# Performance work log

Hardware: AMD Instinct MI355X
Metric: run time of the kernel (lower is better)

Reference implementation:

```python
import jax, jax.numpy as jnp
import numpy as np

NUM_EXPERTS = 8
TOP_K = 2
HIDDEN = 1024
INTER = 1408
B, S = 2, 1024


def setup_inputs() -> dict:
    key = jax.random.key(0)
    k1, k2, k3, k4, k5 = jax.random.split(key, 5)
    scale = 0.02  # keep activations well-scaled
    return {
        "hidden_states": jax.random.normal(k1, (B, S, HIDDEN), dtype=jnp.float32),
        "gate_w": jax.random.normal(k2, (HIDDEN, NUM_EXPERTS), dtype=jnp.float32) * scale,
        "w_gate": jax.random.normal(k3, (NUM_EXPERTS, HIDDEN, INTER), dtype=jnp.float32) * scale,
        "w_up": jax.random.normal(k4, (NUM_EXPERTS, HIDDEN, INTER), dtype=jnp.float32) * scale,
        "w_down": jax.random.normal(k5, (NUM_EXPERTS, INTER, HIDDEN), dtype=jnp.float32) * scale,
    }


def reference(hidden_states, gate_w, w_gate, w_up, w_down):
    b, s, h = hidden_states.shape
    x = hidden_states.reshape(-1, h)  # [T, H]
    # Router: softmax in fp32, top-k, renormalize over selected experts
    logits = x @ gate_w  # [T, E]
    probs = jax.nn.softmax(logits.astype(jnp.float32), axis=-1)
    rw, sel = jax.lax.top_k(probs, TOP_K)  # [T, K]
    rw = rw / jnp.sum(rw, axis=-1, keepdims=True)
    rw = rw.astype(x.dtype)
    # Per-(token, expert) combine weight; duplicates summed (matches torch mask sum)
    combine = jnp.sum(rw[:, :, None] * jax.nn.one_hot(sel, NUM_EXPERTS, dtype=x.dtype), axis=1)  # [T, E]
    out = jnp.zeros_like(x)
    for e in range(NUM_EXPERTS):  # fixed small structural loop over experts
        inter = jax.nn.silu(x @ w_gate[e]) * (x @ w_up[e])  # [T, I]
        out = out + (inter @ w_down[e]) * combine[:, e:e + 1]
    return out.reshape(b, s, h)
```

## Files before the change

### kernel.cpp

```cpp
#include <hip/hip_runtime.h>
#include <hip/hip_bf16.h>

#define T_TOKENS 2048
#define HID 1024
#define ISZ 1408
#define NEXP 8
#define TILES_MAX 72

typedef __bf16 bf16x8 __attribute__((ext_vector_type(8)));
typedef __bf16 bf16x4 __attribute__((ext_vector_type(4)));
typedef float  f32x16 __attribute__((ext_vector_type(16)));

__device__ __forceinline__ void gload16(const void* g, void* l) {
    __builtin_amdgcn_global_load_lds(
        (const __attribute__((address_space(1))) void*)g,
        (__attribute__((address_space(3))) void*)l,
        16, 0, 0);
}

#define PIPE_BARRIER(N)                                              \
    asm volatile("s_waitcnt vmcnt(" #N ") lgkmcnt(0)" ::: "memory"); \
    __builtin_amdgcn_sched_barrier(0);                               \
    __builtin_amdgcn_s_barrier();                                    \
    __builtin_amdgcn_sched_barrier(0);

__global__ __launch_bounds__(256) void prep_kernel(
    const float* __restrict__ x, const float* __restrict__ gw,
    int* __restrict__ sel, float* __restrict__ wt, __bf16* __restrict__ xb,
    const float* __restrict__ wg, const float* __restrict__ wu, const float* __restrict__ wd,
    __bf16* __restrict__ wgT, __bf16* __restrict__ wuT, __bf16* __restrict__ wdT)
{
    __shared__ __bf16 tb[2][64][70];
    const int bid = blockIdx.x;
    const int tid = threadIdx.x;

    if (bid < 512) {
        const int wave = tid >> 6;
        const int lane = tid & 63;
        const int t = bid * 4 + wave;
        const float* xr = x + (size_t)t * HID;

        const int c0 = lane * 16;
        float4 v0 = *(const float4*)(xr + c0);
        float4 v1 = *(const float4*)(xr + c0 + 4);
        float4 v2 = *(const float4*)(xr + c0 + 8);
        float4 v3 = *(const float4*)(xr + c0 + 12);
        {
            bf16x8 o0, o1;
            o0[0]=(__bf16)v0.x; o0[1]=(__bf16)v0.y; o0[2]=(__bf16)v0.z; o0[3]=(__bf16)v0.w;
            o0[4]=(__bf16)v1.x; o0[5]=(__bf16)v1.y; o0[6]=(__bf16)v1.z; o0[7]=(__bf16)v1.w;
            o1[0]=(__bf16)v2.x; o1[1]=(__bf16)v2.y; o1[2]=(__bf16)v2.z; o1[3]=(__bf16)v2.w;
            o1[4]=(__bf16)v3.x; o1[5]=(__bf16)v3.y; o1[6]=(__bf16)v3.z; o1[7]=(__bf16)v3.w;
            *(bf16x8*)(xb + (size_t)t * HID + c0) = o0;
            *(bf16x8*)(xb + (size_t)t * HID + c0 + 8) = o1;
        }
        if (bid == 0 && tid < 128) {
            bf16x8 z8;
            #pragma unroll
            for (int j = 0; j < 8; ++j) z8[j] = (__bf16)0.f;
            *(bf16x8*)(xb + (size_t)T_TOKENS * HID + tid * 8) = z8;
        }

        float le[8] = {0.f, 0.f, 0.f, 0.f, 0.f, 0.f, 0.f, 0.f};
        float xv[16];
        xv[0]=v0.x; xv[1]=v0.y; xv[2]=v0.z; xv[3]=v0.w;
        xv[4]=v1.x; xv[5]=v1.y; xv[6]=v1.z; xv[7]=v1.w;
        xv[8]=v2.x; xv[9]=v2.y; xv[10]=v2.z; xv[11]=v2.w;
        xv[12]=v3.x; xv[13]=v3.y; xv[14]=v3.z; xv[15]=v3.w;
        #pragma unroll
        for (int j = 0; j < 16; ++j) {
            const float* gr = gw + (size_t)(c0 + j) * NEXP;
            float4 g0 = *(const float4*)gr;
            float4 g1 = *(const float4*)(gr + 4);
            le[0] += xv[j] * g0.x; le[1] += xv[j] * g0.y;
            le[2] += xv[j] * g0.z; le[3] += xv[j] * g0.w;
            le[4] += xv[j] * g1.x; le[5] += xv[j] * g1.y;
            le[6] += xv[j] * g1.z; le[7] += xv[j] * g1.w;
        }
        #pragma unroll
        for (int d = 1; d < 64; d <<= 1) {
            #pragma unroll
            for (int k = 0; k < 8; ++k) le[k] += __shfl_xor(le[k], d);
        }
        float m = le[0];
        #pragma unroll
        for (int k = 1; k < 8; ++k) m = fmaxf(m, le[k]);
        float pe[8]; float s = 0.f;
        #pragma unroll
        for (int k = 0; k < 8; ++k) { pe[k] = expf(le[k] - m); s += pe[k]; }
        int e1 = 0; float p1 = pe[0];
        #pragma unroll
        for (int k = 1; k < 8; ++k) if (pe[k] > p1) { p1 = pe[k]; e1 = k; }
        int e2 = -1; float p2 = -1.f;
        #pragma unroll
        for (int k = 0; k < 8; ++k) if (k != e1 && pe[k] > p2) { p2 = pe[k]; e2 = k; }
        if (lane == 0) {
            float inv = 1.0f / (p1 + p2);
            sel[t * 2 + 0] = e1; sel[t * 2 + 1] = e2;
            wt[t * 2 + 0] = p1 * inv; wt[t * 2 + 1] = p2 * inv;
        }
        return;
    }

    const int f   = bid - 512;
    const int z   = f / 176;
    const int rem = f % 176;
    const int bx  = rem / 16;
    const int by  = rem & 15;
    const int e   = z & 7;
    const float* in;
    __bf16* out;
    int R, C, rrA, ccA, rrB, ccB;
    if (z < 16) {
        R = HID; C = ISZ;
        rrA = rrB = by * 64;
        ccA = bx * 128; ccB = ccA + 64;
        in  = (z < 8 ? wg : wu)  + (size_t)e * R * C;
        out = (z < 8 ? wgT : wuT) + (size_t)e * R * C;
    } else {
        R = ISZ; C = HID;
        ccA = ccB = by * 64;
        rrA = bx * 128; rrB = rrA + 64;
        in  = wd  + (size_t)e * R * C;
        out = wdT + (size_t)e * R * C;
    }
    const int lr  = tid >> 4;
    const int lc4 = (tid & 15) * 4;

    auto loadcvt = [&](int buf, int rr, int cc) {
        #pragma unroll
        for (int p = 0; p < 4; ++p) {
            float4 v = *(const float4*)(in + (size_t)(rr + p * 16 + lr) * C + cc + lc4);
            bf16x4 w;
            w[0] = (__bf16)v.x; w[1] = (__bf16)v.y; w[2] = (__bf16)v.z; w[3] = (__bf16)v.w;
            *(bf16x4*)&tb[buf][p * 16 + lr][lc4] = w;
        }
    };
    auto storeT = [&](int buf, int rr, int cc) {
        #pragma unroll
        for (int q = 0; q < 2; ++q) {
            const int oc = (tid >> 3) + 32 * q;
            const int vs = (tid & 7) * 8;
            bf16x8 w;
            #pragma unroll
            for (int j = 0; j < 8; ++j) w[j] = tb[buf][vs + j][oc];
            *(bf16x8*)(out + (size_t)(cc + oc) * R + rr + vs) = w;
        }
    };

    loadcvt(0, rrA, ccA);
    __syncthreads();
    loadcvt(1, rrB, ccB);
    storeT(0, rrA, ccA);
    __syncthreads();
    storeT(1, rrB, ccB);
}

__global__ __launch_bounds__(1024) void scan_assign_kernel(
    int* __restrict__ tiles,
    const int* __restrict__ sel, const float* __restrict__ wt,
    int* __restrict__ rtok, float* __restrict__ rwt, int* __restrict__ tok2row)
{
    __shared__ int hist[NEXP];
    __shared__ int soff[NEXP];
    __shared__ int scur[NEXP];
    if (threadIdx.x < NEXP) { hist[threadIdx.x] = 0; scur[threadIdx.x] = 0; }
    __syncthreads();
    for (int t = threadIdx.x; t < T_TOKENS; t += 1024) {
        atomicAdd(&hist[sel[t * 2 + 0]], 1);
        atomicAdd(&hist[sel[t * 2 + 1]], 1);
    }
    __syncthreads();
    if (threadIdx.x == 0) {
        int cur = 0, tix = 0;
        for (int e = 0; e < NEXP; ++e) {
            soff[e] = cur;
            int n64 = (hist[e] + 63) & ~63;
            for (int rt = 0; rt * 64 < n64; ++rt)
                tiles[tix++] = (e << 16) | (cur + rt * 64);
            cur += n64;
        }
        for (; tix < TILES_MAX; ++tix) tiles[tix] = -1;
    }
    __syncthreads();
    for (int t = threadIdx.x; t < T_TOKENS; t += 1024) {
        #pragma unroll
        for (int k = 0; k < 2; ++k) {
            int e = sel[t * 2 + k];
            int pos = atomicAdd(&scur[e], 1);
            int row = soff[e] + pos;
            rtok[row] = t + 1;
            rwt[row] = wt[t * 2 + k];
            tok2row[t * 2 + k] = row;
        }
    }
}

__global__ __launch_bounds__(256) void ffn1_kernel(
    const __bf16* __restrict__ xb, const int* __restrict__ rtok,
    const __bf16* __restrict__ wgT, const __bf16* __restrict__ wuT,
    const int* __restrict__ tiles, __bf16* __restrict__ inter)
{
    const int n  = blockIdx.x;
    const int nn = (n & 7) * 198 + (n >> 3);
    const int i0 = (nn / TILES_MAX) * 64;
    const int tv = tiles[nn % TILES_MAX];
    if (tv < 0) return;
    const int e = tv >> 16;
    const int rowbase = tv & 0xFFFF;

    __shared__ __align__(16) __bf16 sA[4][64][32];
    __shared__ __align__(16) __bf16 sG[4][64][32];
    __shared__ __align__(16) __bf16 sU[4][64][32];

    const int lane = threadIdx.x & 63;
    const int wid  = threadIdx.x >> 6;
    const int wr = wid >> 1, wc = wid & 1;
    const int l31 = lane & 31;
    const int kg  = lane >> 5;

    const int r16 = lane >> 2;
    const int cz  = (((lane & 3) ^ ((r16 >> 1) & 3)) * 8);
    const int rowA = rowbase + wid * 16 + r16;
    const int tokp = rtok[rowA];
    const int src  = tokp ? (tokp - 1) : T_TOKENS;
    const __bf16* A0 = xb + (size_t)src * HID + cz;
    const size_t wb = (size_t)e * ISZ * HID + (size_t)(i0 + wid * 16 + r16) * HID + cz;
    const __bf16* G0 = wgT + wb;
    const __bf16* U0 = wuT + wb;

    f32x16 accG, accU;
    #pragma unroll
    for (int r = 0; r < 16; ++r) { accG[r] = 0.f; accU[r] = 0.f; }

    auto stage = [&](int b, int k0) {
        gload16(A0 + k0, &sA[b][wid * 16][0]);
        gload16(G0 + k0, &sG[b][wid * 16][0]);
        gload16(U0 + k0, &sU[b][wid * 16][0]);
    };
    auto compute = [&](int b) {
        #pragma unroll
        for (int s = 0; s < 2; ++s) {
            const int ch = ((2 * s + kg) ^ ((l31 >> 1) & 3)) * 8;
            bf16x8 a_ = *(const bf16x8*)&sA[b][wr * 32 + l31][ch];
            bf16x8 g_ = *(const bf16x8*)&sG[b][wc * 32 + l31][ch];
            bf16x8 u_ = *(const bf16x8*)&sU[b][wc * 32 + l31][ch];
            __builtin_amdgcn_s_setprio(1);
            accG = __builtin_amdgcn_mfma_f32_32x32x16_bf16(a_, g_, accG, 0, 0, 0);
            accU = __builtin_amdgcn_mfma_f32_32x32x16_bf16(a_, u_, accU, 0, 0, 0);
            __builtin_amdgcn_s_setprio(0);
        }
    };

    const int nIter = HID / 32;
    stage(0, 0);
    stage(1, 32);
    stage(2, 64);
    PIPE_BARRIER(6)
    for (int i = 0; i < nIter; ++i) {
        int ks = (i + 3 < nIter) ? (i + 3) * 32 : 0;
        stage((i + 3) & 3, ks);
        compute(i & 3);
        PIPE_BARRIER(6)
    }

    const int base_row = rowbase + wr * 32;
    #pragma unroll
    for (int r = 0; r < 16; ++r) {
        float g = accG[r];
        float u = accU[r];
        float v = g / (1.0f + __expf(-g)) * u;
        int row = base_row + (r & 3) + 8 * (r >> 2) + 4 * kg;
        inter[(size_t)row * ISZ + i0 + wc * 32 + l31] = (__bf16)v;
    }
}

__global__ __launch_bounds__(256) void ffn2_kernel(
    const __bf16* __restrict__ inter, const __bf16* __restrict__ wdT,
    const float* __restrict__ rwt, const int* __restrict__ tiles,
    float* __restrict__ y)
{
    const int n  = blockIdx.x;
    const int nn = (n & 7) * 72 + (n >> 3);
    const int n0 = (nn / TILES_MAX) * 128;
    const int tv = tiles[nn % TILES_MAX];
    if (tv < 0) return;
    const int e = tv >> 16;
    const int rowbase = tv & 0xFFFF;

    __shared__ __align__(16) __bf16 sA[4][64][32];
    __shared__ __align__(16) __bf16 sB[4][128][32];

    const int lane = threadIdx.x & 63;
    const int wid  = threadIdx.x >> 6;
    const int wr = wid >> 1, wc = wid & 1;
    const int l31 = lane & 31;
    const int kg  = lane >> 5;

    const int r16 = lane >> 2;
    const int cz  = (((lane & 3) ^ ((r16 >> 1) & 3)) * 8);
    const __bf16* A0 = inter + (size_t)(rowbase + wid * 16 + r16) * ISZ + cz;
    const __bf16* B0 = wdT + (size_t)e * HID * ISZ + (size_t)(n0 + wid * 32 + r16) * ISZ + cz;
    const size_t rstepB = (size_t)16 * ISZ;

    f32x16 acc[2];
    #pragma unroll
    for (int q = 0; q < 2; ++q)
        #pragma unroll
        for (int r = 0; r < 16; ++r) acc[q][r] = 0.f;

    auto stage = [&](int b, int k0) {
        gload16(A0 + k0,          &sA[b][wid * 16][0]);
        gload16(B0 + k0,          &sB[b][wid * 32][0]);
        gload16(B0 + k0 + rstepB, &sB[b][wid * 32 + 16][0]);
    };
    auto compute = [&](int b) {
        #pragma unroll
        for (int s = 0; s < 2; ++s) {
            const int ch = ((2 * s + kg) ^ ((l31 >> 1) & 3)) * 8;
            bf16x8 a_ = *(const bf16x8*)&sA[b][wr * 32 + l31][ch];
            bf16x8 b0 = *(const bf16x8*)&sB[b][wc * 64 + l31][ch];
            bf16x8 b1 = *(const bf16x8*)&sB[b][wc * 64 + 32 + l31][ch];
            __builtin_amdgcn_s_setprio(1);
            acc[0] = __builtin_amdgcn_mfma_f32_32x32x16_bf16(a_, b0, acc[0], 0, 0, 0);
            acc[1] = __builtin_amdgcn_mfma_f32_32x32x16_bf16(a_, b1, acc[1], 0, 0, 0);
            __builtin_amdgcn_s_setprio(0);
        }
    };

    const int nIter = ISZ / 32;
    stage(0, 0);
    stage(1, 32);
    stage(2, 64);
    PIPE_BARRIER(6)
    for (int i = 0; i < nIter; ++i) {
        int ks = (i + 3 < nIter) ? (i + 3) * 32 : 0;
        stage((i + 3) & 3, ks);
        compute(i & 3);
        PIPE_BARRIER(6)
    }

    const int base_row = rowbase + wr * 32;
    #pragma unroll
    for (int q = 0; q < 2; ++q) {
        const int col = n0 + wc * 64 + q * 32 + l31;
        #pragma unroll
        for (int r = 0; r < 16; ++r) {
            int row = base_row + (r & 3) + 8 * (r >> 2) + 4 * kg;
            y[(size_t)row * HID + col] = rwt[row] * acc[q][r];
        }
    }
}

__global__ __launch_bounds__(256) void combine_kernel(
    const float* __restrict__ y, const int* __restrict__ tok2row, float* __restrict__ out)
{
    const int idx = blockIdx.x * 256 + threadIdx.x;
    const int t = idx >> 8;
    const int c = (idx & 255) * 4;
    const int r0 = tok2row[t * 2];
    const int r1 = tok2row[t * 2 + 1];
    float4 a = *(const float4*)(y + (size_t)r0 * HID + c);
    float4 b = *(const float4*)(y + (size_t)r1 * HID + c);
    float4 o = {a.x + b.x, a.y + b.y, a.z + b.z, a.w + b.w};
    *(float4*)(out + (size_t)t * HID + c) = o;
}

extern "C" void kernel_launch(void* const* d_in, const int* in_sizes, int n_in,
                              void* d_out, int out_size, void* d_ws, size_t ws_size,
                              hipStream_t stream) {
    const float* x  = (const float*)d_in[0];
    const float* gw = (const float*)d_in[1];
    const float* wg = (const float*)d_in[2];
    const float* wu = (const float*)d_in[3];
    const float* wd = (const float*)d_in[4];
    float* out = (float*)d_out;

    char* ws = (char*)d_ws;
    int*    tiles   = (int*)(ws + 64);
    int*    sel     = (int*)(ws + 1024);
    float*  wtp     = (float*)(ws + 17408);
    int*    rtok    = (int*)(ws + 33792);
    float*  rwt     = (float*)(ws + 52224);
    int*    tok2row = (int*)(ws + 70656);
    __bf16* xb      = (__bf16*)(ws + 87040);
    __bf16* inter   = (__bf16*)(ws + 4283648);
    __bf16* wgT     = (__bf16*)(ws + 17260032);
    __bf16* wuT     = (__bf16*)(ws + 40328704);
    __bf16* wdT     = (__bf16*)(ws + 63397376);
    float*  y       = (float*)wgT;

    hipMemsetAsync(ws, 0, 87040, stream);

    prep_kernel<<<4736, 256, 0, stream>>>(x, gw, sel, wtp, xb, wg, wu, wd, wgT, wuT, wdT);
    scan_assign_kernel<<<1, 1024, 0, stream>>>(tiles, sel, wtp, rtok, rwt, tok2row);

    ffn1_kernel<<<22 * TILES_MAX, 256, 0, stream>>>(xb, rtok, wgT, wuT, tiles, inter);
    ffn2_kernel<<<8 * TILES_MAX, 256, 0, stream>>>(inter, wdT, rwt, tiles, y);
    combine_kernel<<<(T_TOKENS * HID / 4) / 256, 256, 0, stream>>>(y, tok2row, out);
}
```

Before: 144.5 us.

## Move w_down conversion into ffn1 launch to overlap with gate/up GEMM

The fp32-to-bf16 transpose of w_down moves out of the prep kernel and runs as extra blocks appended to the ffn1 grid. Its conversion can then overlap with the gate/up expert GEMM instead of sitting on the critical path before routing and scan. ffn1 now uses a single shared char buffer aliased for both roles, and the extra blocks compete with GEMM blocks for bandwidth and CUs.

```diff
diff --git a/kernel.cpp b/kernel.cpp
--- a/kernel.cpp
+++ b/kernel.cpp
@@ -27,8 +27,8 @@
 __global__ __launch_bounds__(256) void prep_kernel(
     const float* __restrict__ x, const float* __restrict__ gw,
     int* __restrict__ sel, float* __restrict__ wt, __bf16* __restrict__ xb,
-    const float* __restrict__ wg, const float* __restrict__ wu, const float* __restrict__ wd,
-    __bf16* __restrict__ wgT, __bf16* __restrict__ wuT, __bf16* __restrict__ wdT)
+    const float* __restrict__ wg, const float* __restrict__ wu,
+    __bf16* __restrict__ wgT, __bf16* __restrict__ wuT)
 {
     __shared__ __bf16 tb[2][64][70];
     const int bid = blockIdx.x;
@@ -108,22 +108,11 @@
     const int bx  = rem / 16;
     const int by  = rem & 15;
     const int e   = z & 7;
-    const float* in;
-    __bf16* out;
-    int R, C, rrA, ccA, rrB, ccB;
-    if (z < 16) {
-        R = HID; C = ISZ;
-        rrA = rrB = by * 64;
-        ccA = bx * 128; ccB = ccA + 64;
-        in  = (z < 8 ? wg : wu)  + (size_t)e * R * C;
-        out = (z < 8 ? wgT : wuT) + (size_t)e * R * C;
-    } else {
-        R = ISZ; C = HID;
-        ccA = ccB = by * 64;
-        rrA = bx * 128; rrB = rrA + 64;
-        in  = wd  + (size_t)e * R * C;
-        out = wdT + (size_t)e * R * C;
-    }
+    const int R = HID, C = ISZ;
+    const float* in = (z < 8 ? wg : wu) + (size_t)e * R * C;
+    __bf16* out = (z < 8 ? wgT : wuT) + (size_t)e * R * C;
+    const int rrA = by * 64, rrB = rrA;
+    const int ccA = bx * 128, ccB = ccA + 64;
     const int lr  = tid >> 4;
     const int lc4 = (tid & 15) * 4;
 
@@ -199,9 +188,62 @@
 __global__ __launch_bounds__(256) void ffn1_kernel(
     const __bf16* __restrict__ xb, const int* __restrict__ rtok,
     const __bf16* __restrict__ wgT, const __bf16* __restrict__ wuT,
-    const int* __restrict__ tiles, __bf16* __restrict__ inter)
+    const int* __restrict__ tiles, __bf16* __restrict__ inter,
+    const float* __restrict__ wd, __bf16* __restrict__ wdT)
 {
-    const int n  = blockIdx.x;
+    __shared__ __align__(16) char smem[49152];
+    const int n   = blockIdx.x;
+    const int tid = threadIdx.x;
+
+    if (n >= 22 * TILES_MAX) {
+        auto tb = (__bf16 (*)[64][70])smem;
+        const int f   = n - 22 * TILES_MAX;
+        const int e   = f / 176;
+        const int rem = f % 176;
+        const int bx  = rem / 16;
+        const int by  = rem & 15;
+        const int R = ISZ, C = HID;
+        const float* in = wd + (size_t)e * R * C;
+        __bf16* out = wdT + (size_t)e * R * C;
+        const int ccA = by * 64, ccB = ccA;
+        const int rrA = bx * 128, rrB = rrA + 64;
+        const int lr  = tid >> 4;
+        const int lc4 = (tid & 15) * 4;
+
+        auto loadcvt = [&](int buf, int rr, int cc) {
+            #pragma unroll
+            for (int p = 0; p < 4; ++p) {
+                float4 v = *(const float4*)(in + (size_t)(rr + p * 16 + lr) * C + cc + lc4);
+                bf16x4 w;
+                w[0] = (__bf16)v.x; w[1] = (__bf16)v.y; w[2] = (__bf16)v.z; w[3] = (__bf16)v.w;
+                *(bf16x4*)&tb[buf][p * 16 + lr][lc4] = w;
+            }
+        };
+        auto storeT = [&](int buf, int rr, int cc) {
+            #pragma unroll
+            for (int q = 0; q < 2; ++q) {
+                const int oc = (tid >> 3) + 32 * q;
+                const int vs = (tid & 7) * 8;
+                bf16x8 w;
+                #pragma unroll
+                for (int j = 0; j < 8; ++j) w[j] = tb[buf][vs + j][oc];
+                *(bf16x8*)(out + (size_t)(cc + oc) * R + rr + vs) = w;
+            }
+        };
+
+        loadcvt(0, rrA, ccA);
+        __syncthreads();
+        loadcvt(1, rrB, ccB);
+        storeT(0, rrA, ccA);
+        __syncthreads();
+        storeT(1, rrB, ccB);
+        return;
+    }
+
+    auto sA = (__bf16 (*)[64][32])(smem);
+    auto sG = (__bf16 (*)[64][32])(smem + 16384);
+    auto sU = (__bf16 (*)[64][32])(smem + 32768);
+
     const int nn = (n & 7) * 198 + (n >> 3);
     const int i0 = (nn / TILES_MAX) * 64;
     const int tv = tiles[nn % TILES_MAX];
@@ -209,12 +251,8 @@
     const int e = tv >> 16;
     const int rowbase = tv & 0xFFFF;
 
-    __shared__ __align__(16) __bf16 sA[4][64][32];
-    __shared__ __align__(16) __bf16 sG[4][64][32];
-    __shared__ __align__(16) __bf16 sU[4][64][32];
-
-    const int lane = threadIdx.x & 63;
-    const int wid  = threadIdx.x >> 6;
+    const int lane = tid & 63;
+    const int wid  = tid >> 6;
     const int wr = wid >> 1, wc = wid & 1;
     const int l31 = lane & 31;
     const int kg  = lane >> 5;
@@ -392,10 +430,11 @@
 
     hipMemsetAsync(ws, 0, 87040, stream);
 
-    prep_kernel<<<4736, 256, 0, stream>>>(x, gw, sel, wtp, xb, wg, wu, wd, wgT, wuT, wdT);
+    prep_kernel<<<3328, 256, 0, stream>>>(x, gw, sel, wtp, xb, wg, wu, wgT, wuT);
     scan_assign_kernel<<<1, 1024, 0, stream>>>(tiles, sel, wtp, rtok, rwt, tok2row);
 
-    ffn1_kernel<<<22 * TILES_MAX, 256, 0, stream>>>(xb, rtok, wgT, wuT, tiles, inter);
+    ffn1_kernel<<<22 * TILES_MAX + 1408, 256, 0, stream>>>(
+        xb, rtok, wgT, wuT, tiles, inter, wd, wdT);
     ffn2_kernel<<<8 * TILES_MAX, 256, 0, stream>>>(inter, wdT, rwt, tiles, y);
     combine_kernel<<<(T_TOKENS * HID / 4) / 256, 256, 0, stream>>>(y, tok2row, out);
 }
```

New measurement: 143.0 us. Within noise of the previous version (-1.0%).
